# Performance work log

Hardware: AMD Instinct MI355X
Metric: run time of the kernel (lower is better)

The kernel has to match this reference:

```python
import jax, jax.numpy as jnp
import numpy as np

IN_F, OUT_F, M, BATCH = 64, 64, 20, 1024


def setup_inputs() -> dict:
    key = jax.random.key(0)
    k1, k2 = jax.random.split(key)
    x = jax.random.normal(k1, (BATCH, IN_F), dtype=jnp.float32)
    # parameters, initialized as in the torch module
    z = jnp.tile(jnp.linspace(-1.5, 1.5, M, dtype=jnp.float32).reshape(1, 1, M), (OUT_F, IN_F, 1))
    q_mu = jax.random.normal(k2, (OUT_F, IN_F, M), dtype=jnp.float32) * 0.05
    q_log_var = jnp.full((OUT_F, IN_F, M), -3.0, dtype=jnp.float32)
    log_scale = jnp.zeros((OUT_F, IN_F), dtype=jnp.float32)
    log_variance = jnp.full((OUT_F, IN_F), -1.0, dtype=jnp.float32)
    return {"x": x, "z": z, "q_mu": q_mu, "q_log_var": q_log_var,
            "log_scale": log_scale, "log_variance": log_variance}


def reference(x, z, q_mu, q_log_var, log_scale, log_variance):
    """SVGP-KAN layer, RBF kernel, deterministic input path (x_var = 1e-6).

    Per edge (o,i): basis-function GP f(x) = sum_m w_m k(x, z_m),
    w_m ~ N(q_mu, q_var), k(x,z) = sig2 * exp(-(x-z)^2 / (2 l^2)).
    Gaussian input x ~ N(mu, v) -> closed-form moments (Psi statistics).
    """
    x_mean = x
    x_var = jnp.full_like(x, 1e-6)

    q_var = jnp.clip(jnp.exp(q_log_var), 1e-5)          # [O,I,M]
    sig2 = jnp.clip(jnp.exp(log_variance), 1e-5)        # [O,I]
    ell = jnp.clip(jnp.exp(log_scale), 0.1)             # [O,I] (rbf min_scale=0.1)

    # broadcast: batch x out x in x inducing
    xm = x_mean[:, None, :, None]                       # [B,1,I,1]
    xv = x_var[:, None, :, None]                        # [B,1,I,1]
    zz = z[None]                                        # [1,O,I,M]
    l2 = (ell * ell)[None, :, :, None]                  # [1,O,I,1]
    s2 = sig2[None, :, :, None]                         # [1,O,I,1]

    d2 = (xm - zz) ** 2                                 # [B,O,I,M]
    den1 = l2 + xv
    psi1 = s2 * jnp.sqrt(l2 / den1) * jnp.exp(-d2 / (2.0 * den1))  # E[k(x,z_m)]
    den2 = l2 + 2.0 * xv
    ek2 = (s2 * s2) * jnp.sqrt(l2 / den2) * jnp.exp(-d2 / den2)     # E[k(x,z_m)^2]

    qm = q_mu[None]                                     # [1,O,I,M]
    qv = q_var[None]
    edge_mean = jnp.sum(psi1 * qm, axis=-1)             # [B,O,I]
    edge_var = jnp.sum(ek2 * (qm * qm + qv) - psi1 * psi1 * (qm * qm), axis=-1)
    edge_var = jnp.clip(edge_var, 0.0)                  # [B,O,I]

    y_mean = edge_mean.sum(axis=2)                      # [B,O]
    y_var = edge_var.sum(axis=2)                        # [B,O]
    return y_mean, y_var
```

## Files before the change

### kernel.cpp

```cpp
#include <hip/hip_runtime.h>
#include <hip/hip_bf16.h>

#define OUT_F 64
#define IN_F 64
#define M_PTS 20
#define BATCH 1024

#if __has_builtin(__builtin_amdgcn_exp2f)
#define EXP2(x) __builtin_amdgcn_exp2f(x)
#else
#define EXP2(x) exp2f(x)
#endif

__device__ unsigned g_cp[OUT_F * M_PTS * IN_F];
__device__ float4   g_aux[OUT_F * IN_F];

static __device__ __forceinline__ unsigned f2bf(float f) {
    union { float f; unsigned u; } v; v.f = f;
    unsigned r = v.u + 0x7fffu + ((v.u >> 16) & 1u);
    return r >> 16;
}
static __device__ __forceinline__ float bflo(unsigned p) {
    union { unsigned u; float f; } v; v.u = p << 16; return v.f;
}
static __device__ __forceinline__ float bfhi(unsigned p) {
    union { unsigned u; float f; } v; v.u = p & 0xffff0000u; return v.f;
}

__global__ __launch_bounds__(256) void prep_kernel(
    const float* __restrict__ z, const float* __restrict__ q_mu,
    const float* __restrict__ q_log_var, const float* __restrict__ log_scale,
    const float* __restrict__ log_variance)
{
    int idx = blockIdx.x * 256 + threadIdx.x;
    if (idx >= OUT_F * M_PTS * IN_F) return;
    int i  = idx & 63;
    int om = idx >> 6;
    int m  = om % M_PTS;
    int o  = om / M_PTS;
    int e  = o * IN_F + i;
    int ge = e * M_PTS + m;

    const float LOG2E = 1.4426950408889634f;
    float ell  = fmaxf(expf(log_scale[e]), 0.1f);
    float l2   = ell * ell;
    float sig2 = fmaxf(expf(log_variance[e]), 1e-5f);
    float den1 = l2 + 1e-6f;
    float den2 = l2 + 2e-6f;
    float c1   = sig2 * sqrtf(l2 / den1);
    float c2   = sig2 * sig2 * sqrtf(l2 / den2);
    float s    = sqrtf(0.5f * LOG2E / den1);

    float qm  = q_mu[ge];
    float qv  = fmaxf(expf(q_log_var[ge]), 1e-5f);
    float qmc = c1 * qm;
    float A   = c2 * (qm * qm + qv);
    float B   = A - qmc * qmc;

    g_cp[idx] = f2bf(qmc) | (f2bf(B) << 16);
    if (m == 0) {
        float z0  = z[ge];
        float z19 = z[e * M_PTS + (M_PTS - 1)];
        float delta = (z19 - z0) * (1.0f / (M_PTS - 1));
        float sd = s * delta;
        g_aux[e] = make_float4(s, s * z0, 2.0f * sd, -(sd * sd));
    }
}

#define BODY(P)                                                              \
    {                                                                        \
        float xb0 = xg[((2 * (P)) << 6) + lane];                             \
        float xb1 = xg[((2 * (P) + 1) << 6) + lane];                         \
        float dx0 = fmaf(s, xb0, -sz0);                                      \
        float dx1 = fmaf(s, xb1, -sz0);                                      \
        float t0  = EXP2(-(dx0 * dx0));                                      \
        float t1  = EXP2(-(dx1 * dx1));                                      \
        float w0  = EXP2(fminf(fmaf(cu1, dx0, cu0), 60.0f));                 \
        float w1  = EXP2(fminf(fmaf(cu1, dx1, cu0), 60.0f));                 \
        float em0 = 0.0f, em1 = 0.0f, ev0 = 0.0f, ev1 = 0.0f;                \
        _Pragma("unroll")                                                    \
        for (int m = 0; m < M_PTS; ++m) {                                    \
            unsigned c = cp[m];                                              \
            float qmc = bflo(c);                                             \
            float B   = bfhi(c);                                             \
            em0 = fmaf(qmc, t0, em0);                                        \
            em1 = fmaf(qmc, t1, em1);                                        \
            ev0 = fmaf(B, t0 * t0, ev0);                                     \
            ev1 = fmaf(B, t1 * t1, ev1);                                     \
            if (m < M_PTS - 1) { t0 *= w0; t1 *= w1; w0 *= v; w1 *= v; }     \
        }                                                                    \
        qa[2 * (P)]     = em0;                                               \
        qa[2 * (P) + 1] = em1;                                               \
        qa[8 + 2 * (P)] = fmaxf(ev0, 0.0f);                                  \
        qa[9 + 2 * (P)] = fmaxf(ev1, 0.0f);                                  \
    }

__global__ __launch_bounds__(64, 8) void gpkan_main(
    const float* __restrict__ x, float* __restrict__ out)
{
    const int blk  = blockIdx.x;
    const int o    = blk >> 7;
    const int bc   = blk & 127;
    const int lane = threadIdx.x;

    float4 aux = g_aux[(o << 6) + lane];
    const float s = aux.x, sz0 = aux.y, cu1 = aux.z, cu0 = aux.w;
    const float v = EXP2(cu0 + cu0);

    unsigned cp[M_PTS];
    #pragma unroll
    for (int m = 0; m < M_PTS; ++m)
        cp[m] = g_cp[((o * M_PTS + m) << 6) + lane];

    const float* __restrict__ xg = x + (bc << 9);

    float qa[16];
    BODY(0) BODY(1) BODY(2) BODY(3)

    const bool s5 = (lane & 32) != 0;
    const bool s4 = (lane & 16) != 0;
    const bool s3 = (lane & 8) != 0;
    const bool s2 = (lane & 4) != 0;

    float k8[8];
    #pragma unroll
    for (int j = 0; j < 8; ++j) {
        float keep = s5 ? qa[j + 8] : qa[j];
        float send = s5 ? qa[j] : qa[j + 8];
        k8[j] = keep + __shfl_xor(send, 32);
    }
    float k4[4];
    #pragma unroll
    for (int j = 0; j < 4; ++j) {
        float keep = s4 ? k8[j + 4] : k8[j];
        float send = s4 ? k8[j] : k8[j + 4];
        k4[j] = keep + __shfl_xor(send, 16);
    }
    float k2[2];
    #pragma unroll
    for (int j = 0; j < 2; ++j) {
        float keep = s3 ? k4[j + 2] : k4[j];
        float send = s3 ? k4[j] : k4[j + 2];
        k2[j] = keep + __shfl_xor(send, 8);
    }
    float k1;
    {
        float keep = s2 ? k2[1] : k2[0];
        float send = s2 ? k2[0] : k2[1];
        k1 = keep + __shfl_xor(send, 4);
    }
    k1 += __shfl_xor(k1, 2);
    k1 += __shfl_xor(k1, 1);

    if ((lane & 3) == 0) {
        int row   = ((lane >> 4) & 1) * 4 + ((lane >> 3) & 1) * 2 + ((lane >> 2) & 1);
        int is_ev = (lane >> 5) & 1;
        int b     = (bc << 3) + row;
        out[is_ev * (BATCH * OUT_F) + b * OUT_F + o] = k1;
    }
}

extern "C" void kernel_launch(void* const* d_in, const int* in_sizes, int n_in,
                              void* d_out, int out_size, void* d_ws, size_t ws_size,
                              hipStream_t stream) {
    const float* x            = (const float*)d_in[0];
    const float* z            = (const float*)d_in[1];
    const float* q_mu         = (const float*)d_in[2];
    const float* q_log_var    = (const float*)d_in[3];
    const float* log_scale    = (const float*)d_in[4];
    const float* log_variance = (const float*)d_in[5];
    float* out = (float*)d_out;

    prep_kernel<<<(OUT_F * M_PTS * IN_F + 255) / 256, 256, 0, stream>>>(
        z, q_mu, q_log_var, log_scale, log_variance);
    gpkan_main<<<128 * OUT_F, 64, 0, stream>>>(x, out);
}
```

Baseline: 22.88 us.

## Fuse parameter prep into main kernel via shared-memory staging

Removes the separate prep kernel and global scratch buffers. Each 512-thread block now computes the bf16-packed coefficients and per-edge aux values for its output feature into shared memory, then eight waves each handle eight batch rows. This drops one kernel launch and the global round trip of the precomputed tables. In exchange the prep work is repeated in each of the 16 blocks per output and the grid is restructured into fewer, larger blocks.

After: 22.26 us. 1.03x faster.

```diff
diff --git a/kernel.cpp b/kernel.cpp
--- a/kernel.cpp
+++ b/kernel.cpp
@@ -5,15 +5,14 @@
 #define IN_F 64
 #define M_PTS 20
 #define BATCH 1024
+#define NEPB (IN_F * M_PTS)
 
 #if __has_builtin(__builtin_amdgcn_exp2f)
 #define EXP2(x) __builtin_amdgcn_exp2f(x)
 #else
 #define EXP2(x) exp2f(x)
 #endif
-
-__device__ unsigned g_cp[OUT_F * M_PTS * IN_F];
-__device__ float4   g_aux[OUT_F * IN_F];
+#define LOG2E 1.4426950408889634f
 
 static __device__ __forceinline__ unsigned f2bf(float f) {
     union { float f; unsigned u; } v; v.f = f;
@@ -25,46 +24,6 @@
 }
 static __device__ __forceinline__ float bfhi(unsigned p) {
     union { unsigned u; float f; } v; v.u = p & 0xffff0000u; return v.f;
-}
-
-__global__ __launch_bounds__(256) void prep_kernel(
-    const float* __restrict__ z, const float* __restrict__ q_mu,
-    const float* __restrict__ q_log_var, const float* __restrict__ log_scale,
-    const float* __restrict__ log_variance)
-{
-    int idx = blockIdx.x * 256 + threadIdx.x;
-    if (idx >= OUT_F * M_PTS * IN_F) return;
-    int i  = idx & 63;
-    int om = idx >> 6;
-    int m  = om % M_PTS;
-    int o  = om / M_PTS;
-    int e  = o * IN_F + i;
-    int ge = e * M_PTS + m;
-
-    const float LOG2E = 1.4426950408889634f;
-    float ell  = fmaxf(expf(log_scale[e]), 0.1f);
-    float l2   = ell * ell;
-    float sig2 = fmaxf(expf(log_variance[e]), 1e-5f);
-    float den1 = l2 + 1e-6f;
-    float den2 = l2 + 2e-6f;
-    float c1   = sig2 * sqrtf(l2 / den1);
-    float c2   = sig2 * sig2 * sqrtf(l2 / den2);
-    float s    = sqrtf(0.5f * LOG2E / den1);
-
-    float qm  = q_mu[ge];
-    float qv  = fmaxf(expf(q_log_var[ge]), 1e-5f);
-    float qmc = c1 * qm;
-    float A   = c2 * (qm * qm + qv);
-    float B   = A - qmc * qmc;
-
-    g_cp[idx] = f2bf(qmc) | (f2bf(B) << 16);
-    if (m == 0) {
-        float z0  = z[ge];
-        float z19 = z[e * M_PTS + (M_PTS - 1)];
-        float delta = (z19 - z0) * (1.0f / (M_PTS - 1));
-        float sd = s * delta;
-        g_aux[e] = make_float4(s, s * z0, 2.0f * sd, -(sd * sd));
-    }
 }
 
 #define BODY(P)                                                              \
@@ -95,24 +54,71 @@
         qa[9 + 2 * (P)] = fmaxf(ev1, 0.0f);                                  \
     }
 
-__global__ __launch_bounds__(64, 8) void gpkan_main(
-    const float* __restrict__ x, float* __restrict__ out)
+__global__ __launch_bounds__(512, 8) void gpkan_fused(
+    const float* __restrict__ x, const float* __restrict__ z,
+    const float* __restrict__ q_mu, const float* __restrict__ q_log_var,
+    const float* __restrict__ log_scale, const float* __restrict__ log_variance,
+    float* __restrict__ out)
 {
-    const int blk  = blockIdx.x;
-    const int o    = blk >> 7;
-    const int bc   = blk & 127;
-    const int lane = threadIdx.x;
+    __shared__ unsigned c_lds[NEPB];
+    __shared__ float4   aux_lds[IN_F];
 
-    float4 aux = g_aux[(o << 6) + lane];
+    const int blk = blockIdx.x;
+    const int o   = blk >> 4;
+    const int bc  = blk & 15;
+    const int tid = threadIdx.x;
+
+    const int base = o * NEPB;
+    #pragma unroll
+    for (int kk = 0; kk < 3; ++kk) {
+        int idx = tid + (kk << 9);
+        if (idx < NEPB) {
+            int i = idx / M_PTS;
+            int m = idx - i * M_PTS;
+            int e = (o << 6) + i;
+
+            float ell  = fmaxf(EXP2(log_scale[e] * LOG2E), 0.1f);
+            float l2   = ell * ell;
+            float sig2 = fmaxf(EXP2(log_variance[e] * LOG2E), 1e-5f);
+            float den1 = l2 + 1e-6f;
+            float den2 = l2 + 2e-6f;
+            float c1   = sig2 * sqrtf(l2 / den1);
+            float c2   = sig2 * sig2 * sqrtf(l2 / den2);
+
+            float qm  = q_mu[base + idx];
+            float qv  = fmaxf(EXP2(q_log_var[base + idx] * LOG2E), 1e-5f);
+            float qmc = c1 * qm;
+            float A   = c2 * (qm * qm + qv);
+            float B   = A - qmc * qmc;
+
+            c_lds[(m << 6) + i] = f2bf(qmc) | (f2bf(B) << 16);
+
+            if (m == 0) {
+                float sE    = sqrtf(0.5f * LOG2E / den1);
+                float z0    = z[base + idx];
+                float z19   = z[base + idx + (M_PTS - 1)];
+                float delta = (z19 - z0) * (1.0f / (M_PTS - 1));
+                float sd    = sE * delta;
+                aux_lds[i]  = make_float4(sE, sE * z0, 2.0f * sd, -(sd * sd));
+            }
+        }
+    }
+    __syncthreads();
+
+    const int lane = tid & 63;
+    const int wv   = __builtin_amdgcn_readfirstlane(tid >> 6);
+
+    float4 aux = aux_lds[lane];
     const float s = aux.x, sz0 = aux.y, cu1 = aux.z, cu0 = aux.w;
     const float v = EXP2(cu0 + cu0);
 
     unsigned cp[M_PTS];
     #pragma unroll
     for (int m = 0; m < M_PTS; ++m)
-        cp[m] = g_cp[((o * M_PTS + m) << 6) + lane];
+        cp[m] = c_lds[(m << 6) + lane];
 
-    const float* __restrict__ xg = x + (bc << 9);
+    const int r0 = (bc << 6) + (wv << 3);
+    const float* __restrict__ xg = x + r0 * IN_F;
 
     float qa[16];
     BODY(0) BODY(1) BODY(2) BODY(3)
@@ -155,7 +161,7 @@
     if ((lane & 3) == 0) {
         int row   = ((lane >> 4) & 1) * 4 + ((lane >> 3) & 1) * 2 + ((lane >> 2) & 1);
         int is_ev = (lane >> 5) & 1;
-        int b     = (bc << 3) + row;
+        int b     = r0 + row;
         out[is_ev * (BATCH * OUT_F) + b * OUT_F + o] = k1;
     }
 }
@@ -171,7 +177,6 @@
     const float* log_variance = (const float*)d_in[5];
     float* out = (float*)d_out;
 
-    prep_kernel<<<(OUT_F * M_PTS * IN_F + 255) / 256, 256, 0, stream>>>(
-        z, q_mu, q_log_var, log_scale, log_variance);
-    gpkan_main<<<128 * OUT_F, 64, 0, stream>>>(x, out);
+    gpkan_fused<<<OUT_F * 16, 512, 0, stream>>>(
+        x, z, q_mu, q_log_var, log_scale, log_variance, out);
 }
```
